# Kernel optimization log

Measured on AMD Instinct MI355X. Metric: run time of the kernel, lower is better.

## Reference

```python
import jax, jax.numpy as jnp
import numpy as np

B, P, S, D, DFF, VOCAB, T = 16, 16, 512, 256, 1024, 5000, 256
EPS = 1e-6

def _layernorm(x, g, b):
    mu = jnp.mean(x, axis=-1, keepdims=True)
    var = jnp.var(x, axis=-1, keepdims=True)
    return (x - mu) * jax.lax.rsqrt(var + EPS) * g + b

def setup_inputs() -> dict:
    key = jax.random.key(0)
    ks = jax.random.split(key, 16)
    nrm = lambda k, shape: (jax.random.normal(k, shape) * 0.02).astype(jnp.float32)
    return {
        'x': jax.random.normal(ks[0], (B, P, D), jnp.float32),
        'y': jax.random.randint(ks[1], (B, P, 1), 0, VOCAB),
        'K': jax.random.normal(ks[2], (B, P, S, D), jnp.float32),
        'V': jax.random.normal(ks[3], (B, P, S, D), jnp.float32),
        'R': jax.random.normal(ks[4], (B, P, S, D), jnp.float32),
        'wq': nrm(ks[5], (D, D)), 'bq': jnp.zeros((D,), jnp.float32),
        'wk': nrm(ks[6], (D, D)), 'bk': jnp.zeros((D,), jnp.float32),
        'wv': nrm(ks[7], (D, D)), 'bv': jnp.zeros((D,), jnp.float32),
        'wo': nrm(ks[8], (D, D)), 'bo': jnp.zeros((D,), jnp.float32),
        'w1': nrm(ks[9], (D, DFF)), 'b1': jnp.zeros((DFF,), jnp.float32),
        'w2': nrm(ks[10], (DFF, D)), 'b2': jnp.zeros((D,), jnp.float32),
        'ln1_g': jnp.ones((D,), jnp.float32), 'ln1_b': jnp.zeros((D,), jnp.float32),
        'ln2_g': jnp.ones((D,), jnp.float32), 'ln2_b': jnp.zeros((D,), jnp.float32),
        'w_out': nrm(ks[11], (D, VOCAB)),
        'sigmas': jnp.array([0.1, 0.1, 0.1, 0.1], jnp.float32),  # sigma_q, sigma_k, sigma_v, sigma_z
        'timestep': T,
    }

def reference(x, y, K, V, R, wq, bq, wk, bk, wv, bv, wo, bo, w1, b1, w2, b2,
              ln1_g, ln1_b, ln2_g, ln2_b, w_out, sigmas, timestep):
    t = timestep
    xq = x[:, :, None, :]                                   # (B,P,1,D)
    q_ = xq @ wq + bq
    k_ = xq @ wk + bk
    v_ = xq @ wv + bv
    nk = jax.random.split(jax.random.key(1234), 5)
    # SMC reparameterized gaussian noise on q,k,v
    q = q_ + sigmas[0] * jax.random.normal(nk[0], q_.shape, q_.dtype)
    k = k_ + sigmas[1] * jax.random.normal(nk[1], k_.shape, k_.dtype)
    v = v_ + sigmas[2] * jax.random.normal(nk[2], v_.shape, v_.dtype)
    noise_q = q - q_
    # write current k,v into timestep slot (== concat(past, k, future))
    K = K.at[:, :, t:t + 1, :].set(k)
    V = V.at[:, :, t:t + 1, :].set(v)
    Kw, Vw = K[:, :, :t + 1, :], V[:, :, :t + 1, :]         # causal window
    logits = jnp.einsum('bpqd,bpsd->bpqs', q, Kw) / jnp.sqrt(jnp.float32(D))
    attn = jax.nn.softmax(logits, axis=-1)                  # (B,P,1,t+1)
    z_ = jnp.einsum('bpqs,bpsd->bpqd', attn, Vw) @ wo + bo
    z = z_ + sigmas[3] * jax.random.normal(nk[3], z_.shape, z_.dtype)
    noise_z = z - z_
    out = _layernorm(z + xq, ln1_g, ln1_b)
    f = jax.nn.relu(out @ w1 + b1) @ w2 + b2
    r = _layernorm(f + out, ln2_g, ln2_b)                   # (B,P,1,D)
    preds = r @ w_out                                       # (B,P,1,VOCAB)
    R = R.at[:, :, t:t + 1, :].set(r)
    # particle weights (classification) + ancestor sampling
    probas = jax.nn.softmax(preds, axis=-1)[:, :, 0, :]     # (B,P,VOCAB)
    w = jnp.take_along_axis(probas, y, axis=-1)[:, :, 0]    # (B,P)
    w_norm = jax.lax.stop_gradient(jax.nn.softmax(w, axis=-1))
    i_t = jax.random.categorical(nk[4], w_norm[:, None, :], shape=(B, P))  # (B,P)
    def resample(params):
        past = jnp.take_along_axis(params[:, :, :t + 1, :], i_t[:, :, None, None], axis=1)
        return jnp.concatenate([past, params[:, :, t + 1:, :]], axis=2)
    K, V, R = resample(K), resample(V), resample(R)
    return (r, attn, noise_q, noise_z, K, V, R)
```

## Files before the change

kernel.cpp:

```cpp
#include <hip/hip_runtime.h>
#include <stdint.h>
#include <stddef.h>


#define B_    16
#define P_    16
#define S_    512
#define D_    256
#define DFF_  1024
#define VOCAB_ 5000
#define T_    256
#define ROWS_ 256
#define EPS_  1e-6f

#define PARTITIONABLE 1

__host__ __device__ __forceinline__ uint32_t rotl32_(uint32_t x, int d) {
  return (x << d) | (x >> (32 - d));
}

__host__ __device__ __forceinline__ void threefry2x32_(uint32_t k0, uint32_t k1,
                                                       uint32_t x0, uint32_t x1,
                                                       uint32_t& o0, uint32_t& o1) {
  uint32_t ks2 = k0 ^ k1 ^ 0x1BD11BDAu;
  x0 += k0; x1 += k1;
  x0 += x1; x1 = rotl32_(x1, 13); x1 ^= x0;
  x0 += x1; x1 = rotl32_(x1, 15); x1 ^= x0;
  x0 += x1; x1 = rotl32_(x1, 26); x1 ^= x0;
  x0 += x1; x1 = rotl32_(x1,  6); x1 ^= x0;
  x0 += k1; x1 += ks2 + 1u;
  x0 += x1; x1 = rotl32_(x1, 17); x1 ^= x0;
  x0 += x1; x1 = rotl32_(x1, 29); x1 ^= x0;
  x0 += x1; x1 = rotl32_(x1, 16); x1 ^= x0;
  x0 += x1; x1 = rotl32_(x1, 24); x1 ^= x0;
  x0 += ks2; x1 += k0 + 2u;
  x0 += x1; x1 = rotl32_(x1, 13); x1 ^= x0;
  x0 += x1; x1 = rotl32_(x1, 15); x1 ^= x0;
  x0 += x1; x1 = rotl32_(x1, 26); x1 ^= x0;
  x0 += x1; x1 = rotl32_(x1,  6); x1 ^= x0;
  x0 += k0; x1 += k1 + 3u;
  x0 += x1; x1 = rotl32_(x1, 17); x1 ^= x0;
  x0 += x1; x1 = rotl32_(x1, 29); x1 ^= x0;
  x0 += x1; x1 = rotl32_(x1, 16); x1 ^= x0;
  x0 += x1; x1 = rotl32_(x1, 24); x1 ^= x0;
  x0 += k1; x1 += ks2 + 4u;
  x0 += x1; x1 = rotl32_(x1, 13); x1 ^= x0;
  x0 += x1; x1 = rotl32_(x1, 15); x1 ^= x0;
  x0 += x1; x1 = rotl32_(x1, 26); x1 ^= x0;
  x0 += x1; x1 = rotl32_(x1,  6); x1 ^= x0;
  x0 += ks2; x1 += k0 + 5u;
  o0 = x0; o1 = x1;
}

__device__ __forceinline__ uint32_t jax_bits(uint32_t k0, uint32_t k1,
                                             uint32_t i) {
#if PARTITIONABLE
  uint32_t o0, o1;
  threefry2x32_(k0, k1, 0u, i, o0, o1);
  return o0 ^ o1;
#else
  return 0u;
#endif
}

__device__ __forceinline__ float bits_to_u01(uint32_t b) {
  return __uint_as_float((b >> 9) | 0x3F800000u) - 1.0f;
}

__device__ __forceinline__ float erfinv32(float x) {
  float w = -log1pf(-x * x);
  float p;
  if (w < 5.0f) {
    w -= 2.5f;
    p = 2.81022636e-08f;
    p = fmaf(p, w, 3.43273939e-07f);
    p = fmaf(p, w, -3.5233877e-06f);
    p = fmaf(p, w, -4.39150654e-06f);
    p = fmaf(p, w, 0.00021858087f);
    p = fmaf(p, w, -0.00125372503f);
    p = fmaf(p, w, -0.00417768164f);
    p = fmaf(p, w, 0.246640727f);
    p = fmaf(p, w, 1.50140941f);
  } else {
    w = sqrtf(w) - 3.0f;
    p = -0.000200214257f;
    p = fmaf(p, w, 0.000100950558f);
    p = fmaf(p, w, 0.00134934322f);
    p = fmaf(p, w, -0.00367342844f);
    p = fmaf(p, w, 0.00573950773f);
    p = fmaf(p, w, -0.0076224613f);
    p = fmaf(p, w, 0.00943887047f);
    p = fmaf(p, w, 1.00167406f);
    p = fmaf(p, w, 2.83297682f);
  }
  return p * x;
}

__device__ __forceinline__ float jax_normal(uint32_t k0, uint32_t k1,
                                            uint32_t i) {
  float u01 = bits_to_u01(jax_bits(k0, k1, i));
  const float lo = -0.99999994f;
  float u = __fadd_rn(__fmul_rn(u01, 2.0f), lo);
  u = fmaxf(lo, u);
  return 1.41421356f * erfinv32(u);
}

__device__ __forceinline__ float jax_gumbel(uint32_t k0, uint32_t k1,
                                            uint32_t i) {
  float u01 = bits_to_u01(jax_bits(k0, k1, i));
  const float tiny = 1.17549435e-38f;
  float u = __fadd_rn(__fmul_rn(u01, 1.0f), tiny);
  u = fmaxf(tiny, u);
  return -logf(-logf(u));
}

__device__ __forceinline__ float blk_sum(float v, float* red, int tid) {
  #pragma unroll
  for (int off = 32; off > 0; off >>= 1) v += __shfl_xor(v, off, 64);
  if ((tid & 63) == 0) red[tid >> 6] = v;
  __syncthreads();
  if (tid == 0) {
    float s = 0.f;
    #pragma unroll
    for (int i = 0; i < 16; i++) s += red[i];
    red[16] = s;
  }
  __syncthreads();
  float r = red[16];
  __syncthreads();
  return r;
}
__device__ __forceinline__ float blk_max(float v, float* red, int tid) {
  #pragma unroll
  for (int off = 32; off > 0; off >>= 1) v = fmaxf(v, __shfl_xor(v, off, 64));
  if ((tid & 63) == 0) red[tid >> 6] = v;
  __syncthreads();
  if (tid == 0) {
    float s = -INFINITY;
    #pragma unroll
    for (int i = 0; i < 16; i++) s = fmaxf(s, red[i]);
    red[16] = s;
  }
  __syncthreads();
  float r = red[16];
  __syncthreads();
  return r;
}

__global__ __launch_bounds__(1024) void fused_row_kernel(
    const float* __restrict__ x,
    const float* __restrict__ Kin, const float* __restrict__ Vin,
    const float* __restrict__ wq, const float* __restrict__ bq,
    const float* __restrict__ wk, const float* __restrict__ bk,
    const float* __restrict__ wv, const float* __restrict__ bv,
    const float* __restrict__ wo, const float* __restrict__ bo,
    const float* __restrict__ w1, const float* __restrict__ b1,
    const float* __restrict__ w2, const float* __restrict__ b2,
    const float* __restrict__ ln1g, const float* __restrict__ ln1b,
    const float* __restrict__ ln2g, const float* __restrict__ ln2b,
    const float* __restrict__ sigmas,
    float* __restrict__ kws, float* __restrict__ vws,
    float* __restrict__ attn_out, float* __restrict__ noiseq_out,
    float* __restrict__ noisez_out, float* __restrict__ r_out,
    uint32_t kq0, uint32_t kq1, uint32_t kk0, uint32_t kk1,
    uint32_t kv0, uint32_t kv1, uint32_t kz0, uint32_t kz1) {
  __shared__ __align__(16) float xs[D_], qs[D_], ksh[D_], vsh[D_], z0s[D_], os[D_];
  __shared__ float att[T_ + 4];
  __shared__ __align__(16) float hs[DFF_];
  __shared__ float4 scq[16][64];
  __shared__ float4 sck[16][64];
  __shared__ float4 scv[16][64];
  __shared__ float red[32];
  const int row = blockIdx.x, t = threadIdx.x;
  const int cg = t & 63;
  const int sl = t >> 6;

  if (t < D_) xs[t] = x[row * D_ + t];
  __syncthreads();

  {
    const float4* wqf = (const float4*)wq;
    const float4* wkf = (const float4*)wk;
    const float4* wvf = (const float4*)wv;
    float4 aq = {0,0,0,0}, ak = {0,0,0,0}, av = {0,0,0,0};
    const int e0 = sl * 16;
    #pragma unroll
    for (int e = e0; e < e0 + 16; e++) {
      float xe = xs[e];
      float4 a = wqf[e * 64 + cg];
      float4 b = wkf[e * 64 + cg];
      float4 c = wvf[e * 64 + cg];
      aq.x = fmaf(xe, a.x, aq.x); aq.y = fmaf(xe, a.y, aq.y);
      aq.z = fmaf(xe, a.z, aq.z); aq.w = fmaf(xe, a.w, aq.w);
      ak.x = fmaf(xe, b.x, ak.x); ak.y = fmaf(xe, b.y, ak.y);
      ak.z = fmaf(xe, b.z, ak.z); ak.w = fmaf(xe, b.w, ak.w);
      av.x = fmaf(xe, c.x, av.x); av.y = fmaf(xe, c.y, av.y);
      av.z = fmaf(xe, c.z, av.z); av.w = fmaf(xe, c.w, av.w);
    }
    scq[sl][cg] = aq; sck[sl][cg] = ak; scv[sl][cg] = av;
  }
  __syncthreads();
  if (t < 768) {
    const int m = t >> 8, c = t & 255;
    const float* sc = (m == 0) ? (const float*)scq
                    : (m == 1) ? (const float*)sck : (const float*)scv;
    float s = 0.f;
    #pragma unroll
    for (int j = 0; j < 16; j++) s += sc[j * 256 + c];
    float bias = ((m == 0) ? bq : (m == 1) ? bk : bv)[c];
    float base = bias + s;
    uint32_t i = (uint32_t)row * D_ + c;
    uint32_t a0 = (m == 0) ? kq0 : (m == 1) ? kk0 : kv0;
    uint32_t a1 = (m == 0) ? kq1 : (m == 1) ? kk1 : kv1;
    float val = base + sigmas[m] * jax_normal(a0, a1, i);
    if (m == 0)      { qs[c] = val; noiseq_out[i] = val - base; }
    else if (m == 1) { ksh[c] = val; kws[i] = val; }
    else             { vsh[c] = val; vws[i] = val; }
  }
  __syncthreads();

  {
    const int sq = t >> 2;
    const int qp = t & 3;
    const float4* qf4 = (const float4*)qs;
    const float4* Krow = (const float4*)(Kin + ((size_t)row * S_ + sq) * D_);
    float rr = 0.f;
    #pragma unroll
    for (int j = 0; j < 16; j++) {
      float4 k4 = Krow[j * 4 + qp];
      float4 q4 = qf4[j * 4 + qp];
      rr += q4.x * k4.x + q4.y * k4.y + q4.z * k4.z + q4.w * k4.w;
    }
    rr += __shfl_xor(rr, 1, 64);
    rr += __shfl_xor(rr, 2, 64);
    if (qp == 0) att[sq] = rr * 0.0625f;
    if (t < 64) {
      float4 k4 = ((const float4*)ksh)[t];
      float4 q4 = qf4[t];
      float r2 = q4.x * k4.x + q4.y * k4.y + q4.z * k4.z + q4.w * k4.w;
      #pragma unroll
      for (int off = 32; off > 0; off >>= 1) r2 += __shfl_xor(r2, off, 64);
      if (t == 0) att[T_] = r2 * 0.0625f;
    }
  }
  __syncthreads();

  {
    float v = (t <= T_) ? att[t] : -INFINITY;
    float mx = blk_max(v, red, t);
    float e = (t <= T_) ? expf(att[t] - mx) : 0.f;
    float sum = blk_sum(e, red, t);
    if (t <= T_) {
      float a = e / sum;
      att[t] = a;
      attn_out[(size_t)row * (T_ + 1) + t] = a;
    }
  }
  __syncthreads();

  {
    const float4* Vf = (const float4*)(Vin + (size_t)row * S_ * D_);
    float4 acc = {0,0,0,0};
    const int s0 = sl * 16;
    #pragma unroll
    for (int s = s0; s < s0 + 16; s++) {
      float a = att[s];
      float4 v4 = Vf[s * 64 + cg];
      acc.x = fmaf(a, v4.x, acc.x); acc.y = fmaf(a, v4.y, acc.y);
      acc.z = fmaf(a, v4.z, acc.z); acc.w = fmaf(a, v4.w, acc.w);
    }
    scq[sl][cg] = acc;
  }
  __syncthreads();
  if (t < D_) {
    float s = 0.f;
    #pragma unroll
    for (int j = 0; j < 16; j++) s += ((const float*)scq)[j * 256 + t];
    z0s[t] = s + att[T_] * vsh[t];
  }
  __syncthreads();

  {
    const float4* wof = (const float4*)wo;
    float4 acc = {0,0,0,0};
    const int e0 = sl * 16;
    #pragma unroll
    for (int e = e0; e < e0 + 16; e++) {
      float ze = z0s[e];
      float4 w4 = wof[e * 64 + cg];
      acc.x = fmaf(ze, w4.x, acc.x); acc.y = fmaf(ze, w4.y, acc.y);
      acc.z = fmaf(ze, w4.z, acc.z); acc.w = fmaf(ze, w4.w, acc.w);
    }
    sck[sl][cg] = acc;
  }
  __syncthreads();
  if (t < D_) {
    float s = 0.f;
    #pragma unroll
    for (int j = 0; j < 16; j++) s += ((const float*)sck)[j * 256 + t];
    float zp = bo[t] + s;
    uint32_t i = (uint32_t)row * D_ + t;
    float zn = zp + sigmas[3] * jax_normal(kz0, kz1, i);
    noisez_out[i] = zn - zp;
    z0s[t] = zn + xs[t];
  }
  __syncthreads();
  {
    float y = (t < D_) ? z0s[t] : 0.f;
    float mu = blk_sum(y, red, t) * (1.0f / 256.0f);
    float dv = (t < D_) ? (z0s[t] - mu) : 0.f;
    float var = blk_sum(dv * dv, red, t) * (1.0f / 256.0f);
    if (t < D_) os[t] = dv * rsqrtf(var + EPS_) * ln1g[t] + ln1b[t];
  }
  __syncthreads();

  {
    const int cg8 = t & 255, es = t >> 8;
    const float4* w1f = (const float4*)w1;
    float4 acc = {0,0,0,0};
    const int e0 = es * 64;
    #pragma unroll 8
    for (int e = e0; e < e0 + 64; e++) {
      float oe = os[e];
      float4 w4 = w1f[e * 256 + cg8];
      acc.x = fmaf(oe, w4.x, acc.x); acc.y = fmaf(oe, w4.y, acc.y);
      acc.z = fmaf(oe, w4.z, acc.z); acc.w = fmaf(oe, w4.w, acc.w);
    }
    ((float4*)scq)[es * 256 + cg8] = acc;
  }
  __syncthreads();
  {
    float s = 0.f;
    #pragma unroll
    for (int j = 0; j < 4; j++) s += ((const float*)scq)[j * 1024 + t];
    hs[t] = fmaxf(b1[t] + s, 0.f);
  }
  __syncthreads();

  {
    const float4* w2f = (const float4*)w2;
    float4 acc = {0,0,0,0};
    const int e0 = sl * 64;
    #pragma unroll 8
    for (int e = e0; e < e0 + 64; e++) {
      float he = hs[e];
      float4 w4 = w2f[e * 64 + cg];
      acc.x = fmaf(he, w4.x, acc.x); acc.y = fmaf(he, w4.y, acc.y);
      acc.z = fmaf(he, w4.z, acc.z); acc.w = fmaf(he, w4.w, acc.w);
    }
    scv[sl][cg] = acc;
  }
  __syncthreads();
  if (t < D_) {
    float s = 0.f;
    #pragma unroll
    for (int j = 0; j < 16; j++) s += ((const float*)scv)[j * 256 + t];
    z0s[t] = b2[t] + s + os[t];
  }
  __syncthreads();
  {
    float y = (t < D_) ? z0s[t] : 0.f;
    float mu = blk_sum(y, red, t) * (1.0f / 256.0f);
    float dv = (t < D_) ? (z0s[t] - mu) : 0.f;
    float var = blk_sum(dv * dv, red, t) * (1.0f / 256.0f);
    if (t < D_)
      r_out[(size_t)row * D_ + t] = dv * rsqrtf(var + EPS_) * ln2g[t] + ln2b[t];
  }
}

__global__ __launch_bounds__(256) void preds_kernel(
    const float* __restrict__ r, const float* __restrict__ w_out,
    float* __restrict__ preds) {
  int tid = threadIdx.x;
  int col = blockIdx.x * 250 + tid;
  int rb = blockIdx.y * 16;
  if (tid >= 250) return;
  float acc[16];
  #pragma unroll
  for (int m = 0; m < 16; m++) acc[m] = 0.f;
  #pragma unroll 4
  for (int e = 0; e < D_; e++) {
    float wv = w_out[(size_t)e * VOCAB_ + col];
    #pragma unroll
    for (int m = 0; m < 16; m++)
      acc[m] = fmaf(r[(size_t)(rb + m) * D_ + e], wv, acc[m]);
  }
  #pragma unroll
  for (int m = 0; m < 16; m++)
    preds[(size_t)(rb + m) * VOCAB_ + col] = acc[m];
}

__device__ __forceinline__ float red256_sum(float v, float* red, int tid) {
  red[tid] = v; __syncthreads();
  #pragma unroll
  for (int st = 128; st > 0; st >>= 1) {
    if (tid < st) red[tid] += red[tid + st];
    __syncthreads();
  }
  float r = red[0]; __syncthreads();
  return r;
}
__device__ __forceinline__ float red256_max(float v, float* red, int tid) {
  red[tid] = v; __syncthreads();
  #pragma unroll
  for (int st = 128; st > 0; st >>= 1) {
    if (tid < st) red[tid] = fmaxf(red[tid], red[tid + st]);
    __syncthreads();
  }
  float r = red[0]; __syncthreads();
  return r;
}

__global__ __launch_bounds__(256) void pick_kernel(
    const float* __restrict__ preds, const int* __restrict__ y,
    float* __restrict__ w) {
  __shared__ float red[256];
  int row = blockIdx.x, tid = threadIdx.x;
  const float* pr = preds + (size_t)row * VOCAB_;
  float m = -INFINITY;
  for (int j = tid; j < VOCAB_; j += 256) m = fmaxf(m, pr[j]);
  float mx = red256_max(m, red, tid);
  float s = 0.f;
  for (int j = tid; j < VOCAB_; j += 256) s += expf(pr[j] - mx);
  float sum = red256_sum(s, red, tid);
  if (tid == 0) w[row] = expf(pr[y[row]] - mx) / sum;
}

__global__ __launch_bounds__(256) void cat_kernel(
    const float* __restrict__ w, int* __restrict__ i_t,
    uint32_t kc0, uint32_t kc1) {
  __shared__ float wv[256];
  __shared__ float wn[256];
  int tid = threadIdx.x;
  int b = tid >> 4;
  wv[tid] = w[tid];
  __syncthreads();
  float mx = -INFINITY;
  for (int j = 0; j < 16; j++) mx = fmaxf(mx, wv[b * 16 + j]);
  float ev = expf(wv[tid] - mx);
  wn[tid] = ev;
  __syncthreads();
  float sum = 0.f;
  for (int j = 0; j < 16; j++) sum += wn[b * 16 + j];
  __syncthreads();
  wn[tid] = ev / sum;
  __syncthreads();
  float best = -INFINITY;
  int bi = 0;
  for (int j = 0; j < 16; j++) {
    uint32_t idx = (uint32_t)tid * 16u + (uint32_t)j;
    float g = jax_gumbel(kc0, kc1, idx);
    float sc = g + wn[b * 16 + j];
    if (sc > best) { best = sc; bi = j; }
  }
  i_t[tid] = bi;
}

__global__ __launch_bounds__(256) void resample_kernel(
    const float4* __restrict__ Kin, const float4* __restrict__ Vin,
    const float4* __restrict__ Rin,
    const float4* __restrict__ knew, const float4* __restrict__ vnew,
    const float4* __restrict__ rnew,
    const int* __restrict__ i_t,
    float4* __restrict__ Kout, float4* __restrict__ Vout,
    float4* __restrict__ Rout) {
  uint32_t idx = blockIdx.x * 256u + threadIdx.x;
  uint32_t d4 = idx & 63u;
  uint32_t s  = (idx >> 6) & 511u;
  uint32_t p  = (idx >> 15) & 15u;
  uint32_t b  = idx >> 19;
  const float4* in; const float4* nw; float4* out;
  if (blockIdx.y == 0)      { in = Kin; nw = knew; out = Kout; }
  else if (blockIdx.y == 1) { in = Vin; nw = vnew; out = Vout; }
  else                      { in = Rin; nw = rnew; out = Rout; }
  float4 val;
  if (s > T_) {
    val = in[idx];
  } else {
    uint32_t ip = (uint32_t)i_t[(b << 4) | p];
    if (s == T_) val = nw[(((b << 4) | ip) << 6) | d4];
    else         val = in[(((((b << 4) | ip) << 9) | s) << 6) | d4];
  }
  out[idx] = val;
}

static void compute_subkeys(uint32_t nk[5][2]) {
  const uint32_t k0 = 0u, k1 = 1234u;
  for (uint32_t j = 0; j < 5; j++)
    threefry2x32_(k0, k1, 0u, j, nk[j][0], nk[j][1]);
}

extern "C" void kernel_launch(void* const* d_in, const int* in_sizes, int n_in,
                              void* d_out, int out_size, void* d_ws, size_t ws_size,
                              hipStream_t stream) {
  const float* x    = (const float*)d_in[0];
  const int*   y    = (const int*)d_in[1];
  const float* Kin  = (const float*)d_in[2];
  const float* Vin  = (const float*)d_in[3];
  const float* Rin  = (const float*)d_in[4];
  const float* wq   = (const float*)d_in[5];  const float* bq = (const float*)d_in[6];
  const float* wk   = (const float*)d_in[7];  const float* bk = (const float*)d_in[8];
  const float* wv   = (const float*)d_in[9];  const float* bv = (const float*)d_in[10];
  const float* wo   = (const float*)d_in[11]; const float* bo = (const float*)d_in[12];
  const float* w1   = (const float*)d_in[13]; const float* b1 = (const float*)d_in[14];
  const float* w2   = (const float*)d_in[15]; const float* b2 = (const float*)d_in[16];
  const float* ln1g = (const float*)d_in[17]; const float* ln1b = (const float*)d_in[18];
  const float* ln2g = (const float*)d_in[19]; const float* ln2b = (const float*)d_in[20];
  const float* w_out = (const float*)d_in[21];
  const float* sigmas = (const float*)d_in[22];
  (void)in_sizes; (void)n_in; (void)out_size; (void)ws_size;

  float* out        = (float*)d_out;
  float* r_out      = out;
  float* attn_out   = out + 65536;
  float* noiseq_out = out + 131328;
  float* noisez_out = out + 196864;
  float* K_out      = out + 262400;
  float* V_out      = out + 33816832;
  float* R_out      = out + 67371264;

  float* wsf   = (float*)d_ws;
  float* kws   = wsf;
  float* vws   = wsf + 65536;
  float* preds = wsf + 131072;
  float* wprob = wsf + 1411072;
  int*   i_t   = (int*)(wsf + 1411328);

  uint32_t nk[5][2];
  compute_subkeys(nk);

  fused_row_kernel<<<ROWS_, 1024, 0, stream>>>(
      x, Kin, Vin, wq, bq, wk, bk, wv, bv, wo, bo, w1, b1, w2, b2,
      ln1g, ln1b, ln2g, ln2b, sigmas,
      kws, vws, attn_out, noiseq_out, noisez_out, r_out,
      nk[0][0], nk[0][1], nk[1][0], nk[1][1], nk[2][0], nk[2][1],
      nk[3][0], nk[3][1]);
  preds_kernel<<<dim3(20, 16), 256, 0, stream>>>(r_out, w_out, preds);
  pick_kernel<<<ROWS_, 256, 0, stream>>>(preds, y, wprob);
  cat_kernel<<<1, 256, 0, stream>>>(wprob, i_t, nk[4][0], nk[4][1]);
  resample_kernel<<<dim3(32768, 3), 256, 0, stream>>>(
      (const float4*)Kin, (const float4*)Vin, (const float4*)Rin,
      (const float4*)kws, (const float4*)vws, (const float4*)r_out,
      i_t, (float4*)K_out, (float4*)V_out, (float4*)R_out);
}
```

Baseline: 264.8 us.

## Fuse vocab softmax partials into preds GEMM and overlap tail copy with it

The preds kernel now computes per-block partial max, sum-exp and target-exp values, so the full preds matrix is never written out and read back. A combine step merges these partials inside the categorical sampling kernel. The resample copy of slots after the timestep does not depend on ancestor indices, so it is moved into extra blocks of the preds launch to overlap the memory-bound copy with the GEMM. The head resample kernel now only covers slots up to the timestep. This removes one kernel launch and a preds round-trip, at the cost of a more complex combined grid.

```diff
diff --git a/kernel.cpp b/kernel.cpp
--- a/kernel.cpp
+++ b/kernel.cpp
@@ -368,73 +368,122 @@
   }
 }
 
-__global__ __launch_bounds__(256) void preds_kernel(
+#define PREDS_BLOCKS 320
+#define TAIL_BLOCKS_PER_TENSOR 1020
+__global__ __launch_bounds__(256) void preds_tail_kernel(
     const float* __restrict__ r, const float* __restrict__ w_out,
-    float* __restrict__ preds) {
-  int tid = threadIdx.x;
-  int col = blockIdx.x * 250 + tid;
-  int rb = blockIdx.y * 16;
-  if (tid >= 250) return;
+    const int* __restrict__ y,
+    const float4* __restrict__ Kin, const float4* __restrict__ Vin,
+    const float4* __restrict__ Rin,
+    float4* __restrict__ Kout, float4* __restrict__ Vout,
+    float4* __restrict__ Rout,
+    float* __restrict__ pm, float* __restrict__ ps, float* __restrict__ pe) {
+  const int bx = blockIdx.x, tid = threadIdx.x;
+  if (bx >= PREDS_BLOCKS) {
+    const int c = bx - PREDS_BLOCKS;
+    const int tau = c / TAIL_BLOCKS_PER_TENSOR;
+    const int c2 = c - tau * TAIL_BLOCKS_PER_TENSOR;
+    const uint32_t s = 257u + (uint32_t)(c2 >> 2);
+    const uint32_t q = (uint32_t)(c2 & 3);
+    const float4* in = (tau == 0) ? Kin : (tau == 1) ? Vin : Rin;
+    float4* out      = (tau == 0) ? Kout : (tau == 1) ? Vout : Rout;
+    #pragma unroll
+    for (int k = 0; k < 16; k++) {
+      uint32_t local = (uint32_t)k * 256u + (uint32_t)tid;
+      uint32_t bp = (q << 6) | (local >> 6);
+      uint32_t d4 = local & 63u;
+      uint32_t f4i = (bp << 15) | (s << 6) | d4;
+      out[f4i] = in[f4i];
+    }
+    return;
+  }
+  __shared__ float sm[16][264];
+  __shared__ float pr16[16][17];
+  __shared__ float pms[16], pss[16], eys[16];
+  __shared__ int yvs[16];
+  const int rc = bx / 20, cc = bx - rc * 20;
+  const int rb = rc * 16;
+  const int col = cc * 250 + tid;
+  const int colc = (col < VOCAB_) ? col : (VOCAB_ - 1);
+  if (tid < 16) { yvs[tid] = y[rb + tid]; eys[tid] = 0.f; }
   float acc[16];
   #pragma unroll
   for (int m = 0; m < 16; m++) acc[m] = 0.f;
   #pragma unroll 4
   for (int e = 0; e < D_; e++) {
-    float wv = w_out[(size_t)e * VOCAB_ + col];
+    float wv = w_out[(size_t)e * VOCAB_ + colc];
     #pragma unroll
     for (int m = 0; m < 16; m++)
       acc[m] = fmaf(r[(size_t)(rb + m) * D_ + e], wv, acc[m]);
   }
+  const bool act = (tid < 250);
   #pragma unroll
-  for (int m = 0; m < 16; m++)
-    preds[(size_t)(rb + m) * VOCAB_ + col] = acc[m];
-}
-
-__device__ __forceinline__ float red256_sum(float v, float* red, int tid) {
-  red[tid] = v; __syncthreads();
-  #pragma unroll
-  for (int st = 128; st > 0; st >>= 1) {
-    if (tid < st) red[tid] += red[tid + st];
-    __syncthreads();
-  }
-  float r = red[0]; __syncthreads();
-  return r;
-}
-__device__ __forceinline__ float red256_max(float v, float* red, int tid) {
-  red[tid] = v; __syncthreads();
-  #pragma unroll
-  for (int st = 128; st > 0; st >>= 1) {
-    if (tid < st) red[tid] = fmaxf(red[tid], red[tid + st]);
-    __syncthreads();
-  }
-  float r = red[0]; __syncthreads();
-  return r;
-}
-
-__global__ __launch_bounds__(256) void pick_kernel(
-    const float* __restrict__ preds, const int* __restrict__ y,
-    float* __restrict__ w) {
-  __shared__ float red[256];
-  int row = blockIdx.x, tid = threadIdx.x;
-  const float* pr = preds + (size_t)row * VOCAB_;
-  float m = -INFINITY;
-  for (int j = tid; j < VOCAB_; j += 256) m = fmaxf(m, pr[j]);
-  float mx = red256_max(m, red, tid);
-  float s = 0.f;
-  for (int j = tid; j < VOCAB_; j += 256) s += expf(pr[j] - mx);
-  float sum = red256_sum(s, red, tid);
-  if (tid == 0) w[row] = expf(pr[y[row]] - mx) / sum;
-}
-
-__global__ __launch_bounds__(256) void cat_kernel(
-    const float* __restrict__ w, int* __restrict__ i_t,
+  for (int m = 0; m < 16; m++) sm[m][tid] = act ? acc[m] : -INFINITY;
+  __syncthreads();
+  {
+    const int rr = tid >> 4, j = tid & 15;
+    float mx = -INFINITY;
+    for (int c = j; c < 256; c += 16) mx = fmaxf(mx, sm[rr][c]);
+    pr16[rr][j] = mx;
+  }
+  __syncthreads();
+  if (tid < 16) {
+    float mx = -INFINITY;
+    #pragma unroll
+    for (int j = 0; j < 16; j++) mx = fmaxf(mx, pr16[tid][j]);
+    pms[tid] = mx;
+  }
+  __syncthreads();
+  {
+    const int rr = tid >> 4, j = tid & 15;
+    float mb = pms[rr];
+    float sum = 0.f;
+    for (int c = j; c < 256; c += 16) sum += expf(sm[rr][c] - mb);
+    pr16[rr][j] = sum;
+  }
+  __syncthreads();
+  if (tid < 16) {
+    float s = 0.f;
+    #pragma unroll
+    for (int j = 0; j < 16; j++) s += pr16[tid][j];
+    pss[tid] = s;
+  }
+  __syncthreads();
+  if (act) {
+    #pragma unroll
+    for (int m = 0; m < 16; m++)
+      if (col == yvs[m]) eys[m] = expf(acc[m] - pms[m]);
+  }
+  __syncthreads();
+  if (tid < 16) {
+    pm[(rb + tid) * 20 + cc] = pms[tid];
+    ps[(rb + tid) * 20 + cc] = pss[tid];
+    pe[(rb + tid) * 20 + cc] = eys[tid];
+  }
+}
+
+__global__ __launch_bounds__(256) void combine_cat_kernel(
+    const float* __restrict__ pm, const float* __restrict__ ps,
+    const float* __restrict__ pe, int* __restrict__ i_t,
     uint32_t kc0, uint32_t kc1) {
   __shared__ float wv[256];
   __shared__ float wn[256];
-  int tid = threadIdx.x;
-  int b = tid >> 4;
-  wv[tid] = w[tid];
-  __syncthreads();
+  const int tid = threadIdx.x;
+  {
+    float M = -INFINITY;
+    #pragma unroll 4
+    for (int c = 0; c < 20; c++) M = fmaxf(M, pm[tid * 20 + c]);
+    float S = 0.f, E = 0.f;
+    #pragma unroll 4
+    for (int c = 0; c < 20; c++) {
+      float sc = expf(pm[tid * 20 + c] - M);
+      S += ps[tid * 20 + c] * sc;
+      E += pe[tid * 20 + c] * sc;
+    }
+    wv[tid] = E / S;
+  }
+  __syncthreads();
+  const int b = tid >> 4;
   float mx = -INFINITY;
   for (int j = 0; j < 16; j++) mx = fmaxf(mx, wv[b * 16 + j]);
   float ev = expf(wv[tid] - mx);
@@ -456,7 +505,8 @@
   i_t[tid] = bi;
 }
 
-__global__ __launch_bounds__(256) void resample_kernel(
+#define HEAD_F4_PER_BP 16448u
+__global__ __launch_bounds__(256) void head_resample_kernel(
     const float4* __restrict__ Kin, const float4* __restrict__ Vin,
     const float4* __restrict__ Rin,
     const float4* __restrict__ knew, const float4* __restrict__ vnew,
@@ -465,23 +515,19 @@
     float4* __restrict__ Kout, float4* __restrict__ Vout,
     float4* __restrict__ Rout) {
   uint32_t idx = blockIdx.x * 256u + threadIdx.x;
-  uint32_t d4 = idx & 63u;
-  uint32_t s  = (idx >> 6) & 511u;
-  uint32_t p  = (idx >> 15) & 15u;
-  uint32_t b  = idx >> 19;
+  uint32_t bp = idx / HEAD_F4_PER_BP;
+  uint32_t rrem = idx - bp * HEAD_F4_PER_BP;
+  uint32_t s = rrem >> 6, d4 = rrem & 63u;
   const float4* in; const float4* nw; float4* out;
   if (blockIdx.y == 0)      { in = Kin; nw = knew; out = Kout; }
   else if (blockIdx.y == 1) { in = Vin; nw = vnew; out = Vout; }
   else                      { in = Rin; nw = rnew; out = Rout; }
+  uint32_t ip = (uint32_t)i_t[bp];
+  uint32_t srcbp = (bp & ~15u) | ip;
   float4 val;
-  if (s > T_) {
-    val = in[idx];
-  } else {
-    uint32_t ip = (uint32_t)i_t[(b << 4) | p];
-    if (s == T_) val = nw[(((b << 4) | ip) << 6) | d4];
-    else         val = in[(((((b << 4) | ip) << 9) | s) << 6) | d4];
-  }
-  out[idx] = val;
+  if (s == T_) val = nw[(srcbp << 6) | d4];
+  else         val = in[(srcbp << 15) | (s << 6) | d4];
+  out[(bp << 15) | (s << 6) | d4] = val;
 }
 
 static void compute_subkeys(uint32_t nk[5][2]) {
@@ -519,12 +565,13 @@
   float* V_out      = out + 33816832;
   float* R_out      = out + 67371264;
 
-  float* wsf   = (float*)d_ws;
-  float* kws   = wsf;
-  float* vws   = wsf + 65536;
-  float* preds = wsf + 131072;
-  float* wprob = wsf + 1411072;
-  int*   i_t   = (int*)(wsf + 1411328);
+  float* wsf  = (float*)d_ws;
+  float* kws  = wsf;
+  float* vws  = wsf + 65536;
+  float* pm   = wsf + 131072;
+  float* ps   = wsf + 136192;
+  float* pe   = wsf + 141312;
+  int*   i_t  = (int*)(wsf + 146432);
 
   uint32_t nk[5][2];
   compute_subkeys(nk);
@@ -535,10 +582,14 @@
       kws, vws, attn_out, noiseq_out, noisez_out, r_out,
       nk[0][0], nk[0][1], nk[1][0], nk[1][1], nk[2][0], nk[2][1],
       nk[3][0], nk[3][1]);
-  preds_kernel<<<dim3(20, 16), 256, 0, stream>>>(r_out, w_out, preds);
-  pick_kernel<<<ROWS_, 256, 0, stream>>>(preds, y, wprob);
-  cat_kernel<<<1, 256, 0, stream>>>(wprob, i_t, nk[4][0], nk[4][1]);
-  resample_kernel<<<dim3(32768, 3), 256, 0, stream>>>(
+  preds_tail_kernel<<<PREDS_BLOCKS + 3 * TAIL_BLOCKS_PER_TENSOR, 256, 0, stream>>>(
+      r_out, w_out, y,
+      (const float4*)Kin, (const float4*)Vin, (const float4*)Rin,
+      (float4*)K_out, (float4*)V_out, (float4*)R_out,
+      pm, ps, pe);
+  combine_cat_kernel<<<1, 256, 0, stream>>>(pm, ps, pe, i_t,
+                                            nk[4][0], nk[4][1]);
+  head_resample_kernel<<<dim3(16448, 3), 256, 0, stream>>>(
       (const float4*)Kin, (const float4*)Vin, (const float4*)Rin,
       (const float4*)kws, (const float4*)vws, (const float4*)r_out,
       i_t, (float4*)K_out, (float4*)V_out, (float4*)R_out);
```

Result: faster. 256.7 us (-3.1%).
